# Kernel optimization log

Measured on AMD Instinct MI355X. Metric: run time of the kernel, lower is better.

The kernel has to match this reference:

```python
import jax, jax.numpy as jnp
import numpy as np

D, NH, DH, L, NCP, TW, NTP = 256, 8, 32, 4, 4, 2, 2
P = NCP + TW * NTP  # points per level per head
SHAPES = np.array([[4, 48, 64], [4, 24, 32], [4, 12, 16], [4, 6, 8]], dtype=np.int64)  # (T, H, W) per level


def _offset_biases():
    # Faithful to _reset_parameters: directional grid init for sampling-offset biases.
    thetas = np.arange(NH, dtype=np.float64) * (2.0 * np.pi / NH)
    grid = np.stack([np.cos(thetas), np.sin(thetas)], -1)
    grid = grid / np.abs(grid).max(-1, keepdims=True)
    curr = np.tile(grid.reshape(NH, 1, 1, 2), (1, L, NCP, 1))
    for i in range(NCP):
        curr[:, :, i, :] *= i + 1
    temp = np.tile(grid.reshape(NH, 1, 1, 1, 2), (1, L, TW, NTP, 1))
    init_offset = 0
    for pos, t in enumerate(range(1, TW + 1)):  # encoder default branch
        if t % 2:
            init_offset += 1
        for i in range(NTP):
            temp[:, :, pos, i, :] *= i + 1 + init_offset
    return curr.reshape(-1).astype(np.float32), temp.reshape(-1).astype(np.float32)


def setup_inputs() -> dict:
    key = jax.random.key(0)
    k = jax.random.split(key, 10)
    sizes = SHAPES[:, 0] * SHAPES[:, 1] * SHAPES[:, 2]
    Len_in = int(sizes.sum())  # 16320
    Lq, N = Len_in, 1
    b_so_np, b_tso_np = _offset_biases()
    return {
        "query": jax.random.normal(k[0], (N, Lq, D), jnp.float32),
        "reference_points": jax.random.uniform(k[1], (N, Lq, L, 2), jnp.float32),
        "temporal_offsets": jax.random.normal(k[2], (Lq, L, TW, 2), jnp.float32) * 0.02,
        "input_flatten": jax.random.normal(k[3], (N, Len_in, D), jnp.float32),
        "input_spatial_shapes": jnp.asarray(SHAPES),
        "input_level_start_index": jnp.asarray(np.concatenate([[0], np.cumsum(sizes)[:-1]]).astype(np.int64)),
        "W_so": jax.random.normal(k[4], (D, NH * L * NCP * 2), jnp.float32) * 0.01,
        "b_so": jnp.asarray(b_so_np),
        "W_tso": jax.random.normal(k[5], (D, NH * L * TW * NTP * 2), jnp.float32) * 0.01,
        "b_tso": jnp.asarray(b_tso_np),
        "W_aw": jax.random.normal(k[6], (D, NH * L * NCP), jnp.float32) * 0.02,
        "b_aw": jnp.zeros((NH * L * NCP,), jnp.float32),
        "W_taw": jax.random.normal(k[7], (D, NH * L * TW * NTP), jnp.float32) * 0.02,
        "b_taw": jnp.zeros((NH * L * TW * NTP,), jnp.float32),
        "W_v": jax.random.normal(k[8], (D, D), jnp.float32) / np.sqrt(D),
        "b_v": jnp.zeros((D,), jnp.float32),
        "W_o": jax.random.normal(k[9], (D, D), jnp.float32) / np.sqrt(D),
        "b_o": jnp.zeros((D,), jnp.float32),
    }


def _deform_core(value, loc, attn):
    # value: (N, Len_in, NH, DH); loc: (N, Lq, NH, L, P, 2) in [0,1]; attn: (N, Lq, NH, L, P)
    N, Lq = loc.shape[0], loc.shape[1]
    out = jnp.zeros((N, NH, Lq, DH), value.dtype)
    start = 0
    for l in range(L):  # small fixed level loop
        t, h, w = (int(s) for s in SHAPES[l])
        th = t * h  # frames stacked vertically -> grid is (T*H, W)
        npix = th * w
        v = value[:, start:start + npix].transpose(0, 2, 1, 3)  # (N, NH, npix, DH)
        # grid_sample semantics, align_corners=False, zero padding
        x = loc[:, :, :, l, :, 0] * w - 0.5
        y = loc[:, :, :, l, :, 1] * th - 0.5
        x0 = jnp.floor(x); y0 = jnp.floor(y)
        lx = x - x0; ly = y - y0
        x0i = x0.astype(jnp.int32); y0i = y0.astype(jnp.int32)

        def corner(xi, yi, wgt):
            inb = (xi >= 0) & (xi < w) & (yi >= 0) & (yi < th)
            idx = jnp.clip(yi, 0, th - 1) * w + jnp.clip(xi, 0, w - 1)  # (N,Lq,NH,P)
            idx = idx.transpose(0, 2, 1, 3).reshape(N, NH, Lq * P, 1)
            g = jnp.take_along_axis(v, idx, axis=2).reshape(N, NH, Lq, P, DH)
            wm = (wgt * inb).transpose(0, 2, 1, 3)  # (N,NH,Lq,P)
            return g * wm[..., None]

        samp = (corner(x0i, y0i, (1 - lx) * (1 - ly))
                + corner(x0i + 1, y0i, lx * (1 - ly))
                + corner(x0i, y0i + 1, (1 - lx) * ly)
                + corner(x0i + 1, y0i + 1, lx * ly))
        a = attn[:, :, :, l].transpose(0, 2, 1, 3)  # (N,NH,Lq,P)
        out = out + (samp * a[..., None]).sum(3)
        start += npix
    return out.transpose(0, 2, 1, 3).reshape(N, Lq, D)


def _forward(query, reference_points, temporal_offsets, input_flatten,
             W_so, b_so, W_tso, b_tso, W_aw, b_aw, W_taw, b_taw, W_v, b_v, W_o, b_o):
    N, Lq, _ = query.shape
    value = (input_flatten @ W_v + b_v).reshape(N, -1, NH, DH)
    cso = (query @ W_so + b_so).reshape(N, Lq, NH, L, NCP, 2)
    tso = (query @ W_tso + b_tso).reshape(N, Lq, NH, L, TW, NTP, 2)
    caw = (query @ W_aw + b_aw).reshape(N, Lq, NH, L * NCP)
    taw = (query @ W_taw + b_taw).reshape(N, Lq, NH, L * TW * NTP)
    aw = jax.nn.softmax(jnp.concatenate([caw, taw], -1), -1)  # joint softmax over curr+temporal
    attn = jnp.concatenate([aw[..., :L * NCP].reshape(N, Lq, NH, L, NCP),
                            aw[..., L * NCP:].reshape(N, Lq, NH, L, TW * NTP)], -1)
    # offset_normalizer = [W, T*H] per level
    norm = jnp.asarray(np.stack([SHAPES[:, 2], SHAPES[:, 0] * SHAPES[:, 1]], -1).astype(np.float32))
    tso_n = temporal_offsets[None, :, None, :, :, None, :] + tso / norm[None, None, None, :, None, None, :]
    tso_n = tso_n.reshape(N, Lq, NH, L, TW * NTP, 2)
    cso_n = cso / norm[None, None, None, :, None, :]
    loc = reference_points[:, :, None, :, None, :] + jnp.concatenate([cso_n, tso_n], 4)  # (N,Lq,NH,L,P,2)
    out = _deform_core(value, loc, attn)
    return out @ W_o + b_o


def reference(query, reference_points, temporal_offsets, input_flatten,
              input_spatial_shapes, input_level_start_index,
              W_so, b_so, W_tso, b_tso, W_aw, b_aw, W_taw, b_taw, W_v, b_v, W_o, b_o):
    return _forward(query, reference_points, temporal_offsets, input_flatten,
                    W_so, b_so, W_tso, b_tso, W_aw, b_aw, W_taw, b_taw, W_v, b_v, W_o, b_o)
```

## Files before the change

### kernel.cpp

```cpp
#include <hip/hip_runtime.h>


typedef unsigned short bfraw;
typedef __attribute__((ext_vector_type(4))) float f32x4;
typedef __attribute__((ext_vector_type(8))) short bf16x8;

__device__ __forceinline__ float bf2f(bfraw u) {
  union { unsigned int i; float f; } v; v.i = ((unsigned int)u) << 16; return v.f;
}
__device__ __forceinline__ bfraw f2bf(float f) {
  union { float f; unsigned int i; } v; v.f = f;
  unsigned int x = v.i;
  return (bfraw)((x + 0x7FFFu + ((x >> 16) & 1u)) >> 16);
}
__device__ __forceinline__ float lo16f(unsigned int w) {
  union { unsigned int i; float f; } v; v.i = w << 16; return v.f;
}
__device__ __forceinline__ float hi16f(unsigned int w) {
  union { unsigned int i; float f; } v; v.i = w & 0xFFFF0000u; return v.f;
}
__device__ __forceinline__ float loadx(const void* p, size_t i, int f32m) {
  if (f32m) return ((const float*)p)[i];
  else      return bf2f(((const bfraw*)p)[i]);
}
__device__ __forceinline__ unsigned pk2(float a, float b) {
  return (unsigned)f2bf(a) | ((unsigned)f2bf(b) << 16);
}

__device__ __forceinline__ int vote_f32(const void* q) {
  const unsigned* p = (const unsigned*)q;
  int cnt = 0;
#pragma unroll
  for (int i = 0; i < 16; ++i) {
    const float a = fabsf(lo16f(p[i]));
    cnt += (a > 0.0009765625f && a < 16.0f) ? 1 : 0;
  }
  return (cnt >= 8) ? 0 : 1;
}

__global__ __launch_bounds__(256) void transpose_k(
    const void* W_v, const void* W_so, const void* W_tso,
    const void* W_aw, const void* W_taw, const void* W_o,
    const void* b_so, const void* b_tso, const void* b_aw, const void* b_taw,
    bfraw* __restrict__ WT, float* __restrict__ bcat, const void* query)
{
  const int f32m = vote_f32(query);
  const int b = blockIdx.x, t = threadIdx.x;
  if (b < 1280) {
    float s;
    if (b < 256)       s = loadx(W_v, (size_t)t * 256 + b, f32m);
    else if (b < 1024) {
      const int rp = b - 256;
      if (rp < 256)      s = loadx(W_so,  (size_t)t * 256 + rp, f32m);
      else if (rp < 512) s = loadx(W_tso, (size_t)t * 256 + (rp - 256), f32m);
      else if (rp < 640) s = loadx(W_aw,  (size_t)t * 128 + (rp - 512), f32m);
      else               s = loadx(W_taw, (size_t)t * 128 + (rp - 640), f32m);
    } else               s = loadx(W_o,  (size_t)t * 256 + (b - 1024), f32m);
    WT[(size_t)b * 256 + t] = f2bf(s);
  } else {
    const int i = (b - 1280) * 256 + t;
    if (i < 768) {
      float s;
      if (i < 256)      s = loadx(b_so,  i, f32m);
      else if (i < 512) s = loadx(b_tso, i - 256, f32m);
      else if (i < 640) s = loadx(b_aw,  i - 512, f32m);
      else              s = loadx(b_taw, i - 640, f32m);
      bcat[i] = s;
    }
  }
}

__global__ __launch_bounds__(256) void gemmVP_k(
    const void* __restrict__ inflat, const void* __restrict__ query,
    const bfraw* __restrict__ WT, const void* __restrict__ b_v,
    const float* __restrict__ bcat,
    bfraw* __restrict__ value, bfraw* __restrict__ proj, int M)
{
  __shared__ bfraw As[128][40];
  __shared__ bfraw Bs[128][40];
  const int f32m = vote_f32(query);
  const int y = blockIdx.y;
  const void* A; bfraw* C; int ldc, wtb, colb, bmode;
  if (y < 2) { A = inflat; C = value; ldc = 256; wtb = y * 128;           colb = y * 128;       bmode = 1; }
  else       { A = query;  C = proj;  ldc = 768; wtb = 256 + (y - 2) * 128; colb = (y - 2) * 128; bmode = 0; }

  const int bm = blockIdx.x * 128;
  const int tid = threadIdx.x;
  const int wave = tid >> 6, lane = tid & 63;
  const int quad = lane >> 4, l16 = lane & 15;
  const int mb = (wave >> 1) * 64, nb = (wave & 1) * 64;
  const int srow = tid >> 1;
  const int sk = (tid & 1) * 16;

  int lr = bm + srow; if (lr >= M) lr = M - 1;
  const size_t aoff = (size_t)lr * 256;

  f32x4 acc[4][4] = {{{0.f}}};

  for (int k0 = 0; k0 < 256; k0 += 32) {
    uint4 pa0, pa1;
    if (f32m) {
      const float* Af = (const float*)A + aoff + (k0 + sk);
      const float4 x0 = ((const float4*)Af)[0];
      const float4 x1 = ((const float4*)Af)[1];
      const float4 x2 = ((const float4*)Af)[2];
      const float4 x3 = ((const float4*)Af)[3];
      pa0.x = pk2(x0.x, x0.y); pa0.y = pk2(x0.z, x0.w);
      pa0.z = pk2(x1.x, x1.y); pa0.w = pk2(x1.z, x1.w);
      pa1.x = pk2(x2.x, x2.y); pa1.y = pk2(x2.z, x2.w);
      pa1.z = pk2(x3.x, x3.y); pa1.w = pk2(x3.z, x3.w);
    } else {
      const bfraw* Ab = (const bfraw*)A + aoff + (k0 + sk);
      pa0 = ((const uint4*)Ab)[0];
      pa1 = ((const uint4*)Ab)[1];
    }
    const bfraw* Bb = WT + (size_t)(wtb + srow) * 256 + (k0 + sk);
    const uint4 pb0 = ((const uint4*)Bb)[0];
    const uint4 pb1 = ((const uint4*)Bb)[1];
    *(uint4*)&As[srow][sk]     = pa0;
    *(uint4*)&As[srow][sk + 8] = pa1;
    *(uint4*)&Bs[srow][sk]     = pb0;
    *(uint4*)&Bs[srow][sk + 8] = pb1;
    __syncthreads();

    bf16x8 af[4], bf[4];
#pragma unroll
    for (int i = 0; i < 4; ++i)
      af[i] = *(const bf16x8*)&As[mb + i * 16 + l16][quad * 8];
#pragma unroll
    for (int j = 0; j < 4; ++j)
      bf[j] = *(const bf16x8*)&Bs[nb + j * 16 + l16][quad * 8];
#pragma unroll
    for (int i = 0; i < 4; ++i)
#pragma unroll
      for (int j = 0; j < 4; ++j)
        acc[i][j] = __builtin_amdgcn_mfma_f32_16x16x32_bf16(af[i], bf[j], acc[i][j], 0, 0, 0);
    __syncthreads();
  }

#pragma unroll
  for (int j = 0; j < 4; ++j) {
    const int col = colb + nb + j * 16 + l16;
    const float bb = bmode ? loadx(b_v, col, f32m) : bcat[col];
#pragma unroll
    for (int i = 0; i < 4; ++i) {
#pragma unroll
      for (int r = 0; r < 4; ++r) {
        const int lrow = bm + mb + i * 16 + quad * 4 + r;
        if (lrow < M) C[(size_t)lrow * ldc + col] = f2bf(acc[i][j][r] + bb);
      }
    }
  }
}

__global__ __launch_bounds__(256) void gemmO_k(
    const bfraw* __restrict__ proj, const bfraw* __restrict__ WT,
    const void* __restrict__ b_o, void* __restrict__ Cout,
    const void* __restrict__ query, int M)
{
  __shared__ bfraw As[128][40];
  __shared__ bfraw Bs[128][40];
  const int f32m = vote_f32(query);
  const int bm = blockIdx.x * 128;
  const int bn = blockIdx.y * 128;
  const int tid = threadIdx.x;
  const int wave = tid >> 6, lane = tid & 63;
  const int quad = lane >> 4, l16 = lane & 15;
  const int mb = (wave >> 1) * 64, nb = (wave & 1) * 64;
  const int srow = tid >> 1;
  const int sk = (tid & 1) * 16;

  int lr = bm + srow; if (lr >= M) lr = M - 1;
  const size_t aoff = (size_t)lr * 768;

  f32x4 acc[4][4] = {{{0.f}}};

  for (int k0 = 0; k0 < 256; k0 += 32) {
    const bfraw* Ab = proj + aoff + (k0 + sk);
    const uint4 pa0 = ((const uint4*)Ab)[0];
    const uint4 pa1 = ((const uint4*)Ab)[1];
    const bfraw* Bb = WT + (size_t)(1024 + bn + srow) * 256 + (k0 + sk);
    const uint4 pb0 = ((const uint4*)Bb)[0];
    const uint4 pb1 = ((const uint4*)Bb)[1];
    *(uint4*)&As[srow][sk]     = pa0;
    *(uint4*)&As[srow][sk + 8] = pa1;
    *(uint4*)&Bs[srow][sk]     = pb0;
    *(uint4*)&Bs[srow][sk + 8] = pb1;
    __syncthreads();

    bf16x8 af[4], bf[4];
#pragma unroll
    for (int i = 0; i < 4; ++i)
      af[i] = *(const bf16x8*)&As[mb + i * 16 + l16][quad * 8];
#pragma unroll
    for (int j = 0; j < 4; ++j)
      bf[j] = *(const bf16x8*)&Bs[nb + j * 16 + l16][quad * 8];
#pragma unroll
    for (int i = 0; i < 4; ++i)
#pragma unroll
      for (int j = 0; j < 4; ++j)
        acc[i][j] = __builtin_amdgcn_mfma_f32_16x16x32_bf16(af[i], bf[j], acc[i][j], 0, 0, 0);
    __syncthreads();
  }

#pragma unroll
  for (int j = 0; j < 4; ++j) {
    const int col = bn + nb + j * 16 + l16;
    const float bb = loadx(b_o, col, f32m);
#pragma unroll
    for (int i = 0; i < 4; ++i) {
#pragma unroll
      for (int r = 0; r < 4; ++r) {
        const int lrow = bm + mb + i * 16 + quad * 4 + r;
        if (lrow < M) {
          const float v = acc[i][j][r] + bb;
          if (f32m) ((float*)Cout)[(size_t)lrow * 256 + col] = v;
          else      ((bfraw*)Cout)[(size_t)lrow * 256 + col] = f2bf(v);
        }
      }
    }
  }
}

__global__ __launch_bounds__(256, 4) void sampler_k(
    bfraw* __restrict__ proj, const bfraw* __restrict__ value,
    const void* __restrict__ refp, const void* __restrict__ toff,
    const void* __restrict__ query)
{
  __shared__ int   s_idx[256][4];
  __shared__ float s_w[256][4];

  const int f32m = vote_f32(query);
  const int h = blockIdx.y;
  const int tid = threadIdx.x;
  const int qi = tid >> 5;
  const int sp = tid & 31;
  const int l = sp >> 3;
  const int p = sp & 7;
  const int qg = blockIdx.x * 8 + qi;

  const int W_i[4]  = {64, 32, 16, 8};
  const int TH_i[4] = {192, 96, 48, 24};
  const int ST_i[4] = {0, 12288, 15360, 16128};
  const float Wf  = (float)W_i[l];
  const float THf = (float)TH_i[l];

  bfraw* prow = proj + (size_t)qg * 768;

  const float logit = (p < 4) ? bf2f(prow[512 + h * 16 + l * 4 + p])
                              : bf2f(prow[640 + h * 16 + l * 4 + (p - 4)]);
  float mx = logit;
#pragma unroll
  for (int m = 16; m >= 1; m >>= 1) mx = fmaxf(mx, __shfl_xor(mx, m));
  const float e = __expf(logit - mx);
  float ssum = e;
#pragma unroll
  for (int m = 16; m >= 1; m >>= 1) ssum += __shfl_xor(ssum, m);
  const float attn = e / ssum;

  const float rx = loadx(refp, (size_t)(qg * 4 + l) * 2 + 0, f32m);
  const float ry = loadx(refp, (size_t)(qg * 4 + l) * 2 + 1, f32m);
  float ox, oy;
  if (p < 4) {
    ox = bf2f(prow[h * 32 + l * 8 + p * 2 + 0]) / Wf;
    oy = bf2f(prow[h * 32 + l * 8 + p * 2 + 1]) / THf;
  } else {
    const int pj = p - 4, tw = pj >> 1, j = pj & 1;
    ox = loadx(toff, (size_t)(qg * 4 + l) * 4 + tw * 2 + 0, f32m) +
         bf2f(prow[256 + h * 32 + l * 8 + tw * 4 + j * 2 + 0]) / Wf;
    oy = loadx(toff, (size_t)(qg * 4 + l) * 4 + tw * 2 + 1, f32m) +
         bf2f(prow[256 + h * 32 + l * 8 + tw * 4 + j * 2 + 1]) / THf;
  }
  const float x = (rx + ox) * Wf - 0.5f;
  const float y = (ry + oy) * THf - 0.5f;
  const float x0f = floorf(x), y0f = floorf(y);
  const float lx = x - x0f, ly = y - y0f;
  const int x0 = (int)x0f, y0 = (int)y0f;
  const int Wg = W_i[l], THg = TH_i[l], ST = ST_i[l];
  const float cwx[2] = {1.f - lx, lx};
  const float cwy[2] = {1.f - ly, ly};
#pragma unroll
  for (int c = 0; c < 4; ++c) {
    const int xi = x0 + (c & 1), yi = y0 + (c >> 1);
    const bool inb = (xi >= 0) & (xi < Wg) & (yi >= 0) & (yi < THg);
    const int xc = min(max(xi, 0), Wg - 1);
    const int yc = min(max(yi, 0), THg - 1);
    s_idx[tid][c] = ST + yc * Wg + xc;
    s_w[tid][c] = inb ? (attn * cwx[c & 1] * cwy[c >> 1]) : 0.f;
  }
  __syncthreads();

  {
    const int pg = sp >> 2;
    const int chq = sp & 3;
    const bfraw* vb = value + h * 32 + chq * 8;
    int   idx[16];
    float ww[16];
#pragma unroll
    for (int pt = 0; pt < 4; ++pt) {
      const int ds = qi * 32 + pg * 4 + pt;
#pragma unroll
      for (int c = 0; c < 4; ++c) { idx[pt * 4 + c] = s_idx[ds][c]; ww[pt * 4 + c] = s_w[ds][c]; }
    }
    uint4 vv[16];
#pragma unroll
    for (int i = 0; i < 16; ++i) vv[i] = *(const uint4*)(vb + (size_t)idx[i] * 256);
    float acc[8] = {};
#pragma unroll
    for (int i = 0; i < 16; ++i) {
      const float w = ww[i]; const uint4 v = vv[i];
      acc[0] += w * lo16f(v.x); acc[1] += w * hi16f(v.x);
      acc[2] += w * lo16f(v.y); acc[3] += w * hi16f(v.y);
      acc[4] += w * lo16f(v.z); acc[5] += w * hi16f(v.z);
      acc[6] += w * lo16f(v.w); acc[7] += w * hi16f(v.w);
    }
#pragma unroll
    for (int m = 4; m <= 16; m <<= 1)
#pragma unroll
      for (int r = 0; r < 8; ++r)
        acc[r] += __shfl_xor(acc[r], m);
    if (pg == 0) {
      uint4 pk;
      pk.x = pk2(acc[0], acc[1]);
      pk.y = pk2(acc[2], acc[3]);
      pk.z = pk2(acc[4], acc[5]);
      pk.w = pk2(acc[6], acc[7]);
      *(uint4*)(prow + h * 32 + chq * 8) = pk;
    }
  }
}

extern "C" void kernel_launch(void* const* d_in, const int* in_sizes, int n_in,
                              void* d_out, int out_size, void* d_ws, size_t ws_size,
                              hipStream_t stream)
{
  const void* query  = d_in[0];
  const void* refp   = d_in[1];
  const void* toff   = d_in[2];
  const void* inflat = d_in[3];
  const void* W_so  = d_in[6];
  const void* b_so  = d_in[7];
  const void* W_tso = d_in[8];
  const void* b_tso = d_in[9];
  const void* W_aw  = d_in[10];
  const void* b_aw  = d_in[11];
  const void* W_taw = d_in[12];
  const void* b_taw = d_in[13];
  const void* W_v   = d_in[14];
  const void* b_v   = d_in[15];
  const void* W_o   = d_in[16];
  const void* b_o   = d_in[17];

  const int Lq = 16320;
  const size_t WT_B   = (size_t)1280 * 256 * 2;
  const size_t BCAT_B = 768 * 4;
  const size_t VAL_B  = (size_t)Lq * 256 * 2;
  bfraw* WT    = (bfraw*)d_ws;
  float* bcat  = (float*)((char*)d_ws + WT_B);
  bfraw* value = (bfraw*)((char*)d_ws + WT_B + BCAT_B);
  bfraw* proj  = (bfraw*)((char*)d_ws + WT_B + BCAT_B + VAL_B);

  const dim3 blk(256);
  transpose_k<<<dim3(1283), blk, 0, stream>>>(W_v, W_so, W_tso, W_aw, W_taw, W_o,
                                              b_so, b_tso, b_aw, b_taw, WT, bcat, query);
  gemmVP_k<<<dim3(128, 8), blk, 0, stream>>>(inflat, query, WT, b_v, bcat, value, proj, Lq);
  sampler_k<<<dim3(Lq / 8, 8), blk, 0, stream>>>(proj, value, refp, toff, query);
  gemmO_k<<<dim3(128, 2), blk, 0, stream>>>(proj, WT, b_o, d_out, query, Lq);
}
```

Measured before the change: 245.9 us.

## Store value projection as head-major fp32 and pre-convert sampler inputs

When the workspace is large enough, the value projection is written as fp32 in a head-major layout, [head][Lq][32], instead of bf16 row-major. This makes each head's value slab contiguous and the sampler's gathers 32-byte fp32 loads with no bf16 unpacking. Reference points and temporal offsets are also pre-converted to fp32 in the prep kernel, so the sampler skips the dtype vote. The cost is twice the value bytes written and gathered, plus extra prep work, and bf16 is kept as a fallback path.

```diff
diff --git a/kernel.cpp b/kernel.cpp
--- a/kernel.cpp
+++ b/kernel.cpp
@@ -38,11 +38,13 @@
   return (cnt >= 8) ? 0 : 1;
 }
 
-__global__ __launch_bounds__(256) void transpose_k(
+__global__ __launch_bounds__(256) void prep_k(
     const void* W_v, const void* W_so, const void* W_tso,
     const void* W_aw, const void* W_taw, const void* W_o,
     const void* b_so, const void* b_tso, const void* b_aw, const void* b_taw,
-    bfraw* __restrict__ WT, float* __restrict__ bcat, const void* query)
+    const void* refp, const void* toff,
+    bfraw* __restrict__ WT, float* __restrict__ bcat,
+    float* __restrict__ refpF, float* __restrict__ toffF, const void* query)
 {
   const int f32m = vote_f32(query);
   const int b = blockIdx.x, t = threadIdx.x;
@@ -57,7 +59,7 @@
       else               s = loadx(W_taw, (size_t)t * 128 + (rp - 640), f32m);
     } else               s = loadx(W_o,  (size_t)t * 256 + (b - 1024), f32m);
     WT[(size_t)b * 256 + t] = f2bf(s);
-  } else {
+  } else if (b < 1283) {
     const int i = (b - 1280) * 256 + t;
     if (i < 768) {
       float s;
@@ -67,6 +69,12 @@
       else              s = loadx(b_taw, i - 640, f32m);
       bcat[i] = s;
     }
+  } else if (b < 1793) {
+    const int i = (b - 1283) * 256 + t;
+    refpF[i] = loadx(refp, i, f32m);
+  } else {
+    const int i = (b - 1793) * 256 + t;
+    toffF[i] = loadx(toff, i, f32m);
   }
 }
 
@@ -74,15 +82,15 @@
     const void* __restrict__ inflat, const void* __restrict__ query,
     const bfraw* __restrict__ WT, const void* __restrict__ b_v,
     const float* __restrict__ bcat,
-    bfraw* __restrict__ value, bfraw* __restrict__ proj, int M)
+    void* __restrict__ valueOut, bfraw* __restrict__ proj, int M, int vf32)
 {
   __shared__ bfraw As[128][40];
   __shared__ bfraw Bs[128][40];
   const int f32m = vote_f32(query);
   const int y = blockIdx.y;
-  const void* A; bfraw* C; int ldc, wtb, colb, bmode;
-  if (y < 2) { A = inflat; C = value; ldc = 256; wtb = y * 128;           colb = y * 128;       bmode = 1; }
-  else       { A = query;  C = proj;  ldc = 768; wtb = 256 + (y - 2) * 128; colb = (y - 2) * 128; bmode = 0; }
+  const void* A; int wtb, colb, bmode;
+  if (y < 2) { A = inflat; wtb = y * 128;             colb = y * 128;       bmode = 1; }
+  else       { A = query;  wtb = 256 + (y - 2) * 128; colb = (y - 2) * 128; bmode = 0; }
 
   const int bm = blockIdx.x * 128;
   const int tid = threadIdx.x;
@@ -147,7 +155,15 @@
 #pragma unroll
       for (int r = 0; r < 4; ++r) {
         const int lrow = bm + mb + i * 16 + quad * 4 + r;
-        if (lrow < M) C[(size_t)lrow * ldc + col] = f2bf(acc[i][j][r] + bb);
+        if (lrow < M) {
+          const float vv = acc[i][j][r] + bb;
+          if (!bmode)
+            proj[(size_t)lrow * 768 + col] = f2bf(vv);
+          else if (vf32)
+            ((float*)valueOut)[((size_t)(col >> 5) * M + lrow) * 32 + (col & 31)] = vv;
+          else
+            ((bfraw*)valueOut)[(size_t)lrow * 256 + col] = f2bf(vv);
+        }
       }
     }
   }
@@ -222,15 +238,17 @@
   }
 }
 
+template<int VF32>
 __global__ __launch_bounds__(256, 4) void sampler_k(
-    bfraw* __restrict__ proj, const bfraw* __restrict__ value,
+    bfraw* __restrict__ proj, const void* __restrict__ value,
     const void* __restrict__ refp, const void* __restrict__ toff,
     const void* __restrict__ query)
 {
   __shared__ int   s_idx[256][4];
   __shared__ float s_w[256][4];
 
-  const int f32m = vote_f32(query);
+  int f32m = 0;
+  if constexpr (!VF32) f32m = vote_f32(query);
   const int h = blockIdx.y;
   const int tid = threadIdx.x;
   const int qi = tid >> 5;
@@ -258,18 +276,30 @@
   for (int m = 16; m >= 1; m >>= 1) ssum += __shfl_xor(ssum, m);
   const float attn = e / ssum;
 
-  const float rx = loadx(refp, (size_t)(qg * 4 + l) * 2 + 0, f32m);
-  const float ry = loadx(refp, (size_t)(qg * 4 + l) * 2 + 1, f32m);
+  float rx, ry;
+  if constexpr (VF32) {
+    rx = ((const float*)refp)[(size_t)(qg * 4 + l) * 2 + 0];
+    ry = ((const float*)refp)[(size_t)(qg * 4 + l) * 2 + 1];
+  } else {
+    rx = loadx(refp, (size_t)(qg * 4 + l) * 2 + 0, f32m);
+    ry = loadx(refp, (size_t)(qg * 4 + l) * 2 + 1, f32m);
+  }
   float ox, oy;
   if (p < 4) {
     ox = bf2f(prow[h * 32 + l * 8 + p * 2 + 0]) / Wf;
     oy = bf2f(prow[h * 32 + l * 8 + p * 2 + 1]) / THf;
   } else {
     const int pj = p - 4, tw = pj >> 1, j = pj & 1;
-    ox = loadx(toff, (size_t)(qg * 4 + l) * 4 + tw * 2 + 0, f32m) +
-         bf2f(prow[256 + h * 32 + l * 8 + tw * 4 + j * 2 + 0]) / Wf;
-    oy = loadx(toff, (size_t)(qg * 4 + l) * 4 + tw * 2 + 1, f32m) +
-         bf2f(prow[256 + h * 32 + l * 8 + tw * 4 + j * 2 + 1]) / THf;
+    float tx, ty;
+    if constexpr (VF32) {
+      tx = ((const float*)toff)[(size_t)(qg * 4 + l) * 4 + tw * 2 + 0];
+      ty = ((const float*)toff)[(size_t)(qg * 4 + l) * 4 + tw * 2 + 1];
+    } else {
+      tx = loadx(toff, (size_t)(qg * 4 + l) * 4 + tw * 2 + 0, f32m);
+      ty = loadx(toff, (size_t)(qg * 4 + l) * 4 + tw * 2 + 1, f32m);
+    }
+    ox = tx + bf2f(prow[256 + h * 32 + l * 8 + tw * 4 + j * 2 + 0]) / Wf;
+    oy = ty + bf2f(prow[256 + h * 32 + l * 8 + tw * 4 + j * 2 + 1]) / THf;
   }
   const float x = (rx + ox) * Wf - 0.5f;
   const float y = (ry + oy) * THf - 0.5f;
@@ -293,7 +323,6 @@
   {
     const int pg = sp >> 2;
     const int chq = sp & 3;
-    const bfraw* vb = value + h * 32 + chq * 8;
     int   idx[16];
     float ww[16];
 #pragma unroll
@@ -302,17 +331,34 @@
 #pragma unroll
       for (int c = 0; c < 4; ++c) { idx[pt * 4 + c] = s_idx[ds][c]; ww[pt * 4 + c] = s_w[ds][c]; }
     }
-    uint4 vv[16];
-#pragma unroll
-    for (int i = 0; i < 16; ++i) vv[i] = *(const uint4*)(vb + (size_t)idx[i] * 256);
     float acc[8] = {};
-#pragma unroll
-    for (int i = 0; i < 16; ++i) {
-      const float w = ww[i]; const uint4 v = vv[i];
-      acc[0] += w * lo16f(v.x); acc[1] += w * hi16f(v.x);
-      acc[2] += w * lo16f(v.y); acc[3] += w * hi16f(v.y);
-      acc[4] += w * lo16f(v.z); acc[5] += w * hi16f(v.z);
-      acc[6] += w * lo16f(v.w); acc[7] += w * hi16f(v.w);
+    if constexpr (VF32) {
+      const char* vbase = (const char*)value + (size_t)h * 16320 * 128;
+      const unsigned cb = (unsigned)(chq << 5);
+#pragma unroll
+      for (int i = 0; i < 16; ++i) {
+        const unsigned off = (((unsigned)idx[i]) << 7) | cb;
+        const float4 a4 = *(const float4*)(vbase + off);
+        const float4 b4 = *(const float4*)(vbase + off + 16);
+        const float w = ww[i];
+        acc[0] += w * a4.x; acc[1] += w * a4.y;
+        acc[2] += w * a4.z; acc[3] += w * a4.w;
+        acc[4] += w * b4.x; acc[5] += w * b4.y;
+        acc[6] += w * b4.z; acc[7] += w * b4.w;
+      }
+    } else {
+      const bfraw* vb = (const bfraw*)value + h * 32 + chq * 8;
+      uint4 vv[16];
+#pragma unroll
+      for (int i = 0; i < 16; ++i) vv[i] = *(const uint4*)(vb + (size_t)idx[i] * 256);
+#pragma unroll
+      for (int i = 0; i < 16; ++i) {
+        const float w = ww[i]; const uint4 v = vv[i];
+        acc[0] += w * lo16f(v.x); acc[1] += w * hi16f(v.x);
+        acc[2] += w * lo16f(v.y); acc[3] += w * hi16f(v.y);
+        acc[4] += w * lo16f(v.z); acc[5] += w * hi16f(v.z);
+        acc[6] += w * lo16f(v.w); acc[7] += w * hi16f(v.w);
+      }
     }
 #pragma unroll
     for (int m = 4; m <= 16; m <<= 1)
@@ -354,16 +400,41 @@
   const int Lq = 16320;
   const size_t WT_B   = (size_t)1280 * 256 * 2;
   const size_t BCAT_B = 768 * 4;
-  const size_t VAL_B  = (size_t)Lq * 256 * 2;
-  bfraw* WT    = (bfraw*)d_ws;
-  float* bcat  = (float*)((char*)d_ws + WT_B);
-  bfraw* value = (bfraw*)((char*)d_ws + WT_B + BCAT_B);
-  bfraw* proj  = (bfraw*)((char*)d_ws + WT_B + BCAT_B + VAL_B);
+  const size_t REFP_B = (size_t)Lq * 8 * 4;
+  const size_t TOFF_B = (size_t)Lq * 16 * 4;
+  const size_t VALF_B = (size_t)8 * Lq * 32 * 4;
+  const size_t VALB_B = (size_t)Lq * 256 * 2;
+  const size_t PROJ_B = (size_t)Lq * 768 * 2;
+
+  const size_t need_f32 = WT_B + BCAT_B + REFP_B + TOFF_B + VALF_B + PROJ_B;
+  const int vf32 = (ws_size >= need_f32) ? 1 : 0;
+
+  char* wp = (char*)d_ws;
+  bfraw* WT   = (bfraw*)wp; wp += WT_B;
+  float* bcat = (float*)wp; wp += BCAT_B;
 
   const dim3 blk(256);
-  transpose_k<<<dim3(1283), blk, 0, stream>>>(W_v, W_so, W_tso, W_aw, W_taw, W_o,
-                                              b_so, b_tso, b_aw, b_taw, WT, bcat, query);
-  gemmVP_k<<<dim3(128, 8), blk, 0, stream>>>(inflat, query, WT, b_v, bcat, value, proj, Lq);
-  sampler_k<<<dim3(Lq / 8, 8), blk, 0, stream>>>(proj, value, refp, toff, query);
-  gemmO_k<<<dim3(128, 2), blk, 0, stream>>>(proj, WT, b_o, d_out, query, Lq);
-}
+  if (vf32) {
+    float* refpF = (float*)wp; wp += REFP_B;
+    float* toffF = (float*)wp; wp += TOFF_B;
+    void*  val   = (void*)wp;  wp += VALF_B;
+    bfraw* proj  = (bfraw*)wp;
+
+    prep_k<<<dim3(2813), blk, 0, stream>>>(W_v, W_so, W_tso, W_aw, W_taw, W_o,
+                                           b_so, b_tso, b_aw, b_taw,
+                                           refp, toff, WT, bcat, refpF, toffF, query);
+    gemmVP_k<<<dim3(128, 8), blk, 0, stream>>>(inflat, query, WT, b_v, bcat, val, proj, Lq, 1);
+    sampler_k<1><<<dim3(Lq / 8, 8), blk, 0, stream>>>(proj, val, refpF, toffF, query);
+    gemmO_k<<<dim3(128, 2), blk, 0, stream>>>(proj, WT, b_o, d_out, query, Lq);
+  } else {
+    void*  val  = (void*)wp; wp += VALB_B;
+    bfraw* proj = (bfraw*)wp;
+
+    prep_k<<<dim3(1283), blk, 0, stream>>>(W_v, W_so, W_tso, W_aw, W_taw, W_o,
+                                           b_so, b_tso, b_aw, b_taw,
+                                           refp, toff, WT, bcat, (float*)val, (float*)val, query);
+    gemmVP_k<<<dim3(128, 8), blk, 0, stream>>>(inflat, query, WT, b_v, bcat, val, proj, Lq, 0);
+    sampler_k<0><<<dim3(Lq / 8, 8), blk, 0, stream>>>(proj, val, refp, toff, query);
+    gemmO_k<<<dim3(128, 2), blk, 0, stream>>>(proj, WT, b_o, d_out, query, Lq);
+  }
+}
```

After: 274.9 us. 1.12x slower.

## Store value tensor head-major and pre-convert reference points and offsets to fp32

Applied to the files above, without the earlier changes.

The value projection GEMM now writes its output head-major ([head][row][32 channels]), so each head's value data sits in one contiguous 64-byte-row region. This is meant to improve cache locality for the sampler's gathers, since each block processes a single head. The prep kernel also converts reference_points and temporal_offsets to fp32 ahead of time, which removes the dtype vote and conversion branches from the sampler. The sampler's shared-memory reads of indices and weights are vectorised, and its address arithmetic uses 32-bit shifts. The head-major stores from the GEMM epilogue are more scattered than the previous row-major writes.

```diff
diff --git a/kernel.cpp b/kernel.cpp
--- a/kernel.cpp
+++ b/kernel.cpp
@@ -38,11 +38,13 @@
   return (cnt >= 8) ? 0 : 1;
 }
 
-__global__ __launch_bounds__(256) void transpose_k(
+__global__ __launch_bounds__(256) void prep_k(
     const void* W_v, const void* W_so, const void* W_tso,
     const void* W_aw, const void* W_taw, const void* W_o,
     const void* b_so, const void* b_tso, const void* b_aw, const void* b_taw,
-    bfraw* __restrict__ WT, float* __restrict__ bcat, const void* query)
+    const void* refp, const void* toff,
+    bfraw* __restrict__ WT, float* __restrict__ bcat,
+    float* __restrict__ refpF, float* __restrict__ toffF, const void* query)
 {
   const int f32m = vote_f32(query);
   const int b = blockIdx.x, t = threadIdx.x;
@@ -57,7 +59,7 @@
       else               s = loadx(W_taw, (size_t)t * 128 + (rp - 640), f32m);
     } else               s = loadx(W_o,  (size_t)t * 256 + (b - 1024), f32m);
     WT[(size_t)b * 256 + t] = f2bf(s);
-  } else {
+  } else if (b < 1283) {
     const int i = (b - 1280) * 256 + t;
     if (i < 768) {
       float s;
@@ -67,6 +69,12 @@
       else              s = loadx(b_taw, i - 640, f32m);
       bcat[i] = s;
     }
+  } else if (b < 1793) {
+    const int i = (b - 1283) * 256 + t;
+    refpF[i] = loadx(refp, i, f32m);
+  } else {
+    const int i = (b - 1793) * 256 + t;
+    toffF[i] = loadx(toff, i, f32m);
   }
 }
 
@@ -74,15 +82,15 @@
     const void* __restrict__ inflat, const void* __restrict__ query,
     const bfraw* __restrict__ WT, const void* __restrict__ b_v,
     const float* __restrict__ bcat,
-    bfraw* __restrict__ value, bfraw* __restrict__ proj, int M)
+    bfraw* __restrict__ valueOut, bfraw* __restrict__ proj, int M)
 {
   __shared__ bfraw As[128][40];
   __shared__ bfraw Bs[128][40];
   const int f32m = vote_f32(query);
   const int y = blockIdx.y;
-  const void* A; bfraw* C; int ldc, wtb, colb, bmode;
-  if (y < 2) { A = inflat; C = value; ldc = 256; wtb = y * 128;           colb = y * 128;       bmode = 1; }
-  else       { A = query;  C = proj;  ldc = 768; wtb = 256 + (y - 2) * 128; colb = (y - 2) * 128; bmode = 0; }
+  const void* A; int wtb, colb, bmode;
+  if (y < 2) { A = inflat; wtb = y * 128;             colb = y * 128;       bmode = 1; }
+  else       { A = query;  wtb = 256 + (y - 2) * 128; colb = (y - 2) * 128; bmode = 0; }
 
   const int bm = blockIdx.x * 128;
   const int tid = threadIdx.x;
@@ -147,7 +155,14 @@
 #pragma unroll
       for (int r = 0; r < 4; ++r) {
         const int lrow = bm + mb + i * 16 + quad * 4 + r;
-        if (lrow < M) C[(size_t)lrow * ldc + col] = f2bf(acc[i][j][r] + bb);
+        if (lrow < M) {
+          const float vv = acc[i][j][r] + bb;
+          if (!bmode)
+            proj[(size_t)lrow * 768 + col] = f2bf(vv);
+          else
+            valueOut[((unsigned)(col >> 5) * (unsigned)M + (unsigned)lrow) * 32u
+                     + (unsigned)(col & 31)] = f2bf(vv);
+        }
       }
     }
   }
@@ -224,13 +239,11 @@
 
 __global__ __launch_bounds__(256, 4) void sampler_k(
     bfraw* __restrict__ proj, const bfraw* __restrict__ value,
-    const void* __restrict__ refp, const void* __restrict__ toff,
-    const void* __restrict__ query)
-{
-  __shared__ int   s_idx[256][4];
-  __shared__ float s_w[256][4];
-
-  const int f32m = vote_f32(query);
+    const float* __restrict__ refp, const float* __restrict__ toff)
+{
+  __shared__ __align__(16) int   s_idx[256][4];
+  __shared__ __align__(16) float s_w[256][4];
+
   const int h = blockIdx.y;
   const int tid = threadIdx.x;
   const int qi = tid >> 5;
@@ -258,17 +271,17 @@
   for (int m = 16; m >= 1; m >>= 1) ssum += __shfl_xor(ssum, m);
   const float attn = e / ssum;
 
-  const float rx = loadx(refp, (size_t)(qg * 4 + l) * 2 + 0, f32m);
-  const float ry = loadx(refp, (size_t)(qg * 4 + l) * 2 + 1, f32m);
+  const float rx = refp[(unsigned)(qg * 4 + l) * 2 + 0];
+  const float ry = refp[(unsigned)(qg * 4 + l) * 2 + 1];
   float ox, oy;
   if (p < 4) {
     ox = bf2f(prow[h * 32 + l * 8 + p * 2 + 0]) / Wf;
     oy = bf2f(prow[h * 32 + l * 8 + p * 2 + 1]) / THf;
   } else {
     const int pj = p - 4, tw = pj >> 1, j = pj & 1;
-    ox = loadx(toff, (size_t)(qg * 4 + l) * 4 + tw * 2 + 0, f32m) +
+    ox = toff[(unsigned)(qg * 4 + l) * 4 + tw * 2 + 0] +
          bf2f(prow[256 + h * 32 + l * 8 + tw * 4 + j * 2 + 0]) / Wf;
-    oy = loadx(toff, (size_t)(qg * 4 + l) * 4 + tw * 2 + 1, f32m) +
+    oy = toff[(unsigned)(qg * 4 + l) * 4 + tw * 2 + 1] +
          bf2f(prow[256 + h * 32 + l * 8 + tw * 4 + j * 2 + 1]) / THf;
   }
   const float x = (rx + ox) * Wf - 0.5f;
@@ -293,18 +306,24 @@
   {
     const int pg = sp >> 2;
     const int chq = sp & 3;
-    const bfraw* vb = value + h * 32 + chq * 8;
+    const char* vb = (const char*)(value + (unsigned)h * (16320u * 32u));
+    const unsigned cb = (unsigned)(chq << 4);
     int   idx[16];
     float ww[16];
 #pragma unroll
     for (int pt = 0; pt < 4; ++pt) {
       const int ds = qi * 32 + pg * 4 + pt;
-#pragma unroll
-      for (int c = 0; c < 4; ++c) { idx[pt * 4 + c] = s_idx[ds][c]; ww[pt * 4 + c] = s_w[ds][c]; }
+      const int4   ia = *(const int4*)&s_idx[ds][0];
+      const float4 wa = *(const float4*)&s_w[ds][0];
+      idx[pt * 4 + 0] = ia.x; idx[pt * 4 + 1] = ia.y;
+      idx[pt * 4 + 2] = ia.z; idx[pt * 4 + 3] = ia.w;
+      ww[pt * 4 + 0] = wa.x; ww[pt * 4 + 1] = wa.y;
+      ww[pt * 4 + 2] = wa.z; ww[pt * 4 + 3] = wa.w;
     }
     uint4 vv[16];
 #pragma unroll
-    for (int i = 0; i < 16; ++i) vv[i] = *(const uint4*)(vb + (size_t)idx[i] * 256);
+    for (int i = 0; i < 16; ++i)
+      vv[i] = *(const uint4*)(vb + ((((unsigned)idx[i]) << 6) | cb));
     float acc[8] = {};
 #pragma unroll
     for (int i = 0; i < 16; ++i) {
@@ -354,16 +373,24 @@
   const int Lq = 16320;
   const size_t WT_B   = (size_t)1280 * 256 * 2;
   const size_t BCAT_B = 768 * 4;
-  const size_t VAL_B  = (size_t)Lq * 256 * 2;
-  bfraw* WT    = (bfraw*)d_ws;
-  float* bcat  = (float*)((char*)d_ws + WT_B);
-  bfraw* value = (bfraw*)((char*)d_ws + WT_B + BCAT_B);
-  bfraw* proj  = (bfraw*)((char*)d_ws + WT_B + BCAT_B + VAL_B);
+  const size_t REFP_B = (size_t)Lq * 8 * 4;
+  const size_t TOFF_B = (size_t)Lq * 16 * 4;
+  const size_t VAL_B  = (size_t)8 * Lq * 32 * 2;
+  (void)ws_size;
+
+  char* wp = (char*)d_ws;
+  bfraw* WT    = (bfraw*)wp; wp += WT_B;
+  float* bcat  = (float*)wp; wp += BCAT_B;
+  float* refpF = (float*)wp; wp += REFP_B;
+  float* toffF = (float*)wp; wp += TOFF_B;
+  bfraw* value = (bfraw*)wp; wp += VAL_B;
+  bfraw* proj  = (bfraw*)wp;
 
   const dim3 blk(256);
-  transpose_k<<<dim3(1283), blk, 0, stream>>>(W_v, W_so, W_tso, W_aw, W_taw, W_o,
-                                              b_so, b_tso, b_aw, b_taw, WT, bcat, query);
+  prep_k<<<dim3(2813), blk, 0, stream>>>(W_v, W_so, W_tso, W_aw, W_taw, W_o,
+                                         b_so, b_tso, b_aw, b_taw,
+                                         refp, toff, WT, bcat, refpF, toffF, query);
   gemmVP_k<<<dim3(128, 8), blk, 0, stream>>>(inflat, query, WT, b_v, bcat, value, proj, Lq);
-  sampler_k<<<dim3(Lq / 8, 8), blk, 0, stream>>>(proj, value, refp, toff, query);
+  sampler_k<<<dim3(Lq / 8, 8), blk, 0, stream>>>(proj, value, refpF, toffF);
   gemmO_k<<<dim3(128, 2), blk, 0, stream>>>(proj, WT, b_o, d_out, query, Lq);
 }
```

Result: faster. 232.7 us (-5.4%).
